# Kernel optimization log

Hardware: AMD Instinct MI355X
Metric: run time of the kernel (lower is better)

## Reference

```python
import jax, jax.numpy as jnp
import numpy as np

NH = 16   # num_heads
HD = 128  # head_dim
HS = 2048 # hidden_size
LI, LT = 2048, 512
MLP = 4 * HS


def _ln(x, s, b):
    m = jnp.mean(x, axis=-1, keepdims=True)
    v = jnp.var(x, axis=-1, keepdims=True)
    return (x - m) * jax.lax.rsqrt(v + 1e-6) * s + b


def _rms(x, s):
    return x * jax.lax.rsqrt(jnp.mean(x * x, axis=-1, keepdims=True) + 1e-6) * s


def _mod6(vec, w, b):
    a = (jax.nn.silu(vec) @ w + b)[:, None, :]
    return jnp.split(a, 6, axis=-1)  # shift1,scale1,gate1,shift2,scale2,gate2


def _rope(x, pe):
    B, H, L, D = x.shape
    xr = x.reshape(B, H, L, D // 2, 1, 2)
    return (pe[..., 0] * xr[..., 0] + pe[..., 1] * xr[..., 1]).reshape(B, H, L, D)


def _attention(q, k, v, pe):
    q = _rope(q, pe)
    k = _rope(k, pe)
    scores = jnp.einsum('bhqd,bhkd->bhqk', q, k) * (q.shape[-1] ** -0.5)
    p = jax.nn.softmax(scores, axis=-1)
    o = jnp.einsum('bhqk,bhkd->bhqd', p, v)
    B, H, L, D = o.shape
    return o.transpose(0, 2, 1, 3).reshape(B, L, H * D)


def _prenorm_qkv(x, shift, scale, ln_s, ln_b, qkv_w, qkv_b, qn, kn):
    xm = (1.0 + scale) * _ln(x, ln_s, ln_b) + shift
    y = xm @ qkv_w + qkv_b
    B, L, _ = y.shape
    y = y.reshape(B, L, 3, NH, HD).transpose(2, 0, 3, 1, 4)  # K B H L D
    q, k, v = y[0], y[1], y[2]
    return _rms(q, qn), _rms(k, kn), v


def _forward(img, txt, vec, pe,
             img_mod_w, img_mod_b, img_norm1_s, img_norm1_b, img_qkv_w, img_qkv_b,
             img_qn_s, img_kn_s, img_proj_w, img_proj_b, img_norm2_s, img_norm2_b,
             img_mlp_w1, img_mlp_b1, img_mlp_w2, img_mlp_b2,
             txt_mod_w, txt_mod_b, txt_norm1_s, txt_norm1_b, txt_qkv_w, txt_qkv_b,
             txt_qn_s, txt_kn_s, txt_proj_w, txt_proj_b, txt_norm2_s, txt_norm2_b,
             txt_mlp_w1, txt_mlp_b1, txt_mlp_w2, txt_mlp_b2):
    i_sh1, i_sc1, i_g1, i_sh2, i_sc2, i_g2 = _mod6(vec, img_mod_w, img_mod_b)
    t_sh1, t_sc1, t_g1, t_sh2, t_sc2, t_g2 = _mod6(vec, txt_mod_w, txt_mod_b)

    iq, ik, iv = _prenorm_qkv(img, i_sh1, i_sc1, img_norm1_s, img_norm1_b,
                              img_qkv_w, img_qkv_b, img_qn_s, img_kn_s)
    tq, tk, tv = _prenorm_qkv(txt, t_sh1, t_sc1, txt_norm1_s, txt_norm1_b,
                              txt_qkv_w, txt_qkv_b, txt_qn_s, txt_kn_s)

    q = jnp.concatenate((tq, iq), axis=2)
    k = jnp.concatenate((tk, ik), axis=2)
    v = jnp.concatenate((tv, iv), axis=2)
    attn = _attention(q, k, v, pe)  # [B, LT+LI, HS]
    Lt = txt.shape[1]
    txt_attn, img_attn = attn[:, :Lt], attn[:, Lt:]

    img = img + i_g1 * (img_attn @ img_proj_w + img_proj_b)
    img_h = (1.0 + i_sc2) * _ln(img, img_norm2_s, img_norm2_b) + i_sh2
    img = img + i_g2 * (jax.nn.gelu(img_h @ img_mlp_w1 + img_mlp_b1) @ img_mlp_w2 + img_mlp_b2)

    txt = txt + t_g1 * (txt_attn @ txt_proj_w + txt_proj_b)
    txt_h = (1.0 + t_sc2) * _ln(txt, txt_norm2_s, txt_norm2_b) + t_sh2
    txt = txt + t_g2 * (jax.nn.gelu(txt_h @ txt_mlp_w1 + txt_mlp_b1) @ txt_mlp_w2 + txt_mlp_b2)
    return img, txt


def setup_inputs() -> dict:
    key = jax.random.key(0)
    ki = iter(jax.random.split(key, 48))
    def n(shape, s=0.02):
        return jax.random.normal(next(ki), shape, jnp.float32) * s
    d = {
        'img': jax.random.normal(next(ki), (1, LI, HS), jnp.float32),
        'txt': jax.random.normal(next(ki), (1, LT, HS), jnp.float32),
        'vec': jax.random.normal(next(ki), (1, HS), jnp.float32),
        'pe': jax.random.normal(next(ki), (1, 1, LT + LI, HD // 2, 2, 2), jnp.float32),
    }
    for p in ('img', 'txt'):
        d[p + '_mod_w'] = n((HS, 6 * HS)); d[p + '_mod_b'] = jnp.zeros((6 * HS,), jnp.float32)
        d[p + '_norm1_s'] = jnp.ones((HS,), jnp.float32); d[p + '_norm1_b'] = jnp.zeros((HS,), jnp.float32)
        d[p + '_qkv_w'] = n((HS, 3 * HS)); d[p + '_qkv_b'] = jnp.zeros((3 * HS,), jnp.float32)
        d[p + '_qn_s'] = jnp.ones((HD,), jnp.float32); d[p + '_kn_s'] = jnp.ones((HD,), jnp.float32)
        d[p + '_proj_w'] = n((HS, HS)); d[p + '_proj_b'] = jnp.zeros((HS,), jnp.float32)
        d[p + '_norm2_s'] = jnp.ones((HS,), jnp.float32); d[p + '_norm2_b'] = jnp.zeros((HS,), jnp.float32)
        d[p + '_mlp_w1'] = n((HS, MLP)); d[p + '_mlp_b1'] = jnp.zeros((MLP,), jnp.float32)
        d[p + '_mlp_w2'] = n((MLP, HS)); d[p + '_mlp_b2'] = jnp.zeros((HS,), jnp.float32)
    return d


def reference(img, txt, vec, pe,
              img_mod_w, img_mod_b, img_norm1_s, img_norm1_b, img_qkv_w, img_qkv_b,
              img_qn_s, img_kn_s, img_proj_w, img_proj_b, img_norm2_s, img_norm2_b,
              img_mlp_w1, img_mlp_b1, img_mlp_w2, img_mlp_b2,
              txt_mod_w, txt_mod_b, txt_norm1_s, txt_norm1_b, txt_qkv_w, txt_qkv_b,
              txt_qn_s, txt_kn_s, txt_proj_w, txt_proj_b, txt_norm2_s, txt_norm2_b,
              txt_mlp_w1, txt_mlp_b1, txt_mlp_w2, txt_mlp_b2):
    return _forward(img, txt, vec, pe,
                    img_mod_w, img_mod_b, img_norm1_s, img_norm1_b, img_qkv_w, img_qkv_b,
                    img_qn_s, img_kn_s, img_proj_w, img_proj_b, img_norm2_s, img_norm2_b,
                    img_mlp_w1, img_mlp_b1, img_mlp_w2, img_mlp_b2,
                    txt_mod_w, txt_mod_b, txt_norm1_s, txt_norm1_b, txt_qkv_w, txt_qkv_b,
                    txt_qn_s, txt_kn_s, txt_proj_w, txt_proj_b, txt_norm2_s, txt_norm2_b,
                    txt_mlp_w1, txt_mlp_b1, txt_mlp_w2, txt_mlp_b2)
```

## Files before the change

kernel.cpp:

```cpp
#include <hip/hip_runtime.h>
#include <hip/hip_bf16.h>
#include <math.h>

typedef __bf16 bf16;
typedef __bf16 bf16x2 __attribute__((ext_vector_type(2)));
typedef __bf16 bf16x4 __attribute__((ext_vector_type(4)));
typedef __bf16 bf16x8 __attribute__((ext_vector_type(8)));
typedef float f32x4 __attribute__((ext_vector_type(4)));

#define HS 2048
#define NH 16
#define HD 128
#define LT 512
#define LI 2048
#define LQ 2560
#define MLP_D 8192
#define SPLIT 4
#define KVS (LQ / SPLIT)
#define KVBLK 32
#define NTILES (KVS / KVBLK)

__device__ __forceinline__ f32x4 mfma16(bf16x8 a, bf16x8 b, f32x4 c) {
  return __builtin_amdgcn_mfma_f32_16x16x32_bf16(a, b, c, 0, 0, 0);
}

__device__ __forceinline__ void gl_lds16(const bf16* g, bf16* l) {
  __builtin_amdgcn_global_load_lds((const __attribute__((address_space(1))) void*)g,
                                   (__attribute__((address_space(3))) void*)l, 16, 0, 0);
}

__global__ void k_silu(const float* __restrict__ v, float* __restrict__ s) {
  int i = blockIdx.x * 256 + threadIdx.x;
  float x = v[i];
  s[i] = x / (1.f + expf(-x));
}

__global__ __launch_bounds__(256) void k_mod_partial(
    const float* __restrict__ s, const float* __restrict__ w_txt,
    const float* __restrict__ w_img, float* __restrict__ part) {
  int strm = blockIdx.x / 48;
  int n = (blockIdx.x % 48) * 256 + threadIdx.x;
  const float* w = strm ? w_img : w_txt;
  int k0 = blockIdx.y * 256;
  __shared__ float sl[256];
  sl[threadIdx.x] = s[k0 + threadIdx.x];
  __syncthreads();
  float acc = 0.f;
  for (int k = 0; k < 256; k++)
    acc += sl[k] * w[(size_t)(k0 + k) * 12288 + n];
  part[((size_t)blockIdx.y * 2 + strm) * 12288 + n] = acc;
}

__global__ __launch_bounds__(256) void k_mod_reduce(
    const float* __restrict__ part, const float* __restrict__ b_txt,
    const float* __restrict__ b_img, float* __restrict__ mod) {
  int strm = blockIdx.x / 48;
  int n = (blockIdx.x % 48) * 256 + threadIdx.x;
  float acc = strm ? b_img[n] : b_txt[n];
  for (int kc = 0; kc < 8; kc++)
    acc += part[((size_t)kc * 2 + strm) * 12288 + n];
  mod[(size_t)strm * 12288 + n] = acc;
}

__global__ __launch_bounds__(256) void k_transpose_cvt(
    const float* __restrict__ src, bf16* __restrict__ dst, int R, int C) {
  __shared__ float t[64][65];
  int tx = threadIdx.x & 63, ty = threadIdx.x >> 6;
  int c0 = blockIdx.x * 64, r0 = blockIdx.y * 64;
  for (int i = 0; i < 64; i += 4)
    t[ty + i][tx] = src[(size_t)(r0 + ty + i) * C + c0 + tx];
  __syncthreads();
#pragma unroll
  for (int j = 0; j < 2; j++) {
    int c = (threadIdx.x >> 3) + j * 32;
    int gg = (threadIdx.x & 7) * 8;
    bf16x8 ov;
#pragma unroll
    for (int k = 0; k < 8; k++) ov[k] = (bf16)t[gg + k][c];
    *(bf16x8*)(dst + (size_t)(c0 + c) * R + r0 + gg) = ov;
  }
}

__global__ __launch_bounds__(256) void k_ln_mod(
    const float* __restrict__ x0, const float* __restrict__ x1,
    const float* __restrict__ ls0, const float* __restrict__ lb0,
    const float* __restrict__ ls1, const float* __restrict__ lb1,
    const float* __restrict__ mod0, const float* __restrict__ mod1,
    int shidx, int scidx, bf16* __restrict__ out) {
  int r = blockIdx.x;
  int strm = r >= LT;
  const float* x = strm ? (x1 + (size_t)(r - LT) * HS) : (x0 + (size_t)r * HS);
  const float* ls = strm ? ls1 : ls0;
  const float* lb = strm ? lb1 : lb0;
  const float* md = strm ? mod1 : mod0;
  const float* sh = md + (size_t)shidx * HS;
  const float* sc = md + (size_t)scidx * HS;
  int t = threadIdx.x;
  float4 a = ((const float4*)x)[t * 2];
  float4 b = ((const float4*)x)[t * 2 + 1];
  float xv[8] = {a.x, a.y, a.z, a.w, b.x, b.y, b.z, b.w};
  float sum = 0.f, sq = 0.f;
#pragma unroll
  for (int j = 0; j < 8; j++) { sum += xv[j]; sq += xv[j] * xv[j]; }
#pragma unroll
  for (int m = 32; m; m >>= 1) { sum += __shfl_xor(sum, m); sq += __shfl_xor(sq, m); }
  __shared__ float red[8];
  int lane = t & 63, wid = t >> 6;
  if (!lane) { red[wid] = sum; red[wid + 4] = sq; }
  __syncthreads();
  float ts = red[0] + red[1] + red[2] + red[3];
  float tq = red[4] + red[5] + red[6] + red[7];
  float mean = ts * (1.f / HS);
  float var = tq * (1.f / HS) - mean * mean;
  float inv = rsqrtf(var + 1e-6f);
  int c0 = t * 8;
  bf16x8 ov;
#pragma unroll
  for (int j = 0; j < 8; j++) {
    int c = c0 + j;
    float v = ((xv[j] - mean) * inv * ls[c] + lb[c]) * (1.f + sc[c]) + sh[c];
    ov[j] = (bf16)v;
  }
  *(bf16x8*)(out + (size_t)r * HS + c0) = ov;
}

template <int MODE>
__global__ __launch_bounds__(256) void k_gemm(
    const bf16* __restrict__ A, int K, int N, int Ksz,
    const bf16* __restrict__ BT0, const bf16* __restrict__ BT1,
    const float* __restrict__ bias0, const float* __restrict__ bias1,
    void* __restrict__ out0, void* __restrict__ out1) {
  __shared__ bf16 As[3][128 * 32];
  __shared__ bf16 Bs[3][128 * 32];
  int tid = threadIdx.x;
  int bn = blockIdx.x, bm = blockIdx.y;
  int strm = (bm * 128) >= LT;
  int lm = bm * 128 - strm * LT;
  const bf16* BT = strm ? BT1 : BT0;
  int lane = tid & 63, wid = tid >> 6;
  int wr = wid >> 1, wc = wid & 1;
  int sc_ = (lane & 7) ^ (lane >> 3);
  int Rb = wid * 16 + 2 * (lane >> 3) + (sc_ >> 2);
  int koff = (sc_ & 3) * 8;
  const bf16* Ag = A + (size_t)(bm * 128 + Rb) * K + koff;
  const bf16* Bg = BT + (size_t)(bn * 128 + Rb) * K + koff;
  int kbeg = MODE == 4 ? blockIdx.z * Ksz : 0;
  int nk = Ksz / 32;
  auto stage = [&](int buf, int ks) {
    int k0 = kbeg + ks * 32;
    gl_lds16(Ag + k0, &As[buf][wid * 512]);
    gl_lds16(Ag + (size_t)64 * K + k0, &As[buf][2048 + wid * 512]);
    gl_lds16(Bg + k0, &Bs[buf][wid * 512]);
    gl_lds16(Bg + (size_t)64 * K + k0, &Bs[buf][2048 + wid * 512]);
  };
  f32x4 acc[4][4] = {};
  int r16 = lane & 15, g = lane >> 4;
  int Lr = r16 >> 1;
  int pf_ = (((r16 & 1) << 2) + g) ^ Lr;
  stage(0, 0);
  if (nk > 1) stage(1, 1);
  int c0 = 0;
  for (int ks = 0; ks < nk; ks++) {
    if (ks + 1 < nk) asm volatile("s_waitcnt vmcnt(4)" ::: "memory");
    else             asm volatile("s_waitcnt vmcnt(0)" ::: "memory");
    __builtin_amdgcn_s_barrier();
    asm volatile("" ::: "memory");
    int c2 = c0 + 2; if (c2 >= 3) c2 -= 3;
    if (ks + 2 < nk) stage(c2, ks + 2);
    bf16x8 af[4], bfr[4];
#pragma unroll
    for (int m = 0; m < 4; m++)
      af[m] = *(const bf16x8*)&As[c0][(wr * 32 + m * 8 + Lr) * 64 + pf_ * 8];
#pragma unroll
    for (int n = 0; n < 4; n++)
      bfr[n] = *(const bf16x8*)&Bs[c0][(wc * 32 + n * 8 + Lr) * 64 + pf_ * 8];
#pragma unroll
    for (int m = 0; m < 4; m++)
#pragma unroll
      for (int n = 0; n < 4; n++)
        acc[m][n] = mfma16(af[m], bfr[n], acc[m][n]);
    c0 = (c0 + 1 == 3) ? 0 : c0 + 1;
  }
  int col = lane & 15, rb = (lane >> 4) * 4;
  const float* bias = strm ? bias1 : bias0;
  float* part = MODE == 4 ? (float*)out0 + (size_t)blockIdx.z * LQ * N : nullptr;
#pragma unroll
  for (int m = 0; m < 4; m++) {
#pragma unroll
    for (int n = 0; n < 4; n++) {
      int gn = bn * 128 + wc * 64 + n * 16 + col;
      float bv = MODE == 4 ? 0.f : bias[gn];
#pragma unroll
      for (int r = 0; r < 4; r++) {
        int lr = wr * 64 + m * 16 + rb + r;
        float v = acc[m][n][r] + bv;
        if (MODE == 0) {
          ((bf16*)(strm ? out1 : out0))[(size_t)(lm + lr) * N + gn] = (bf16)v;
        } else if (MODE == 2) {
          float u2 = 1.5957691216057308f * (v + 0.044715f * v * v * v);
          float ge = v / (1.f + __expf(-u2));
          ((bf16*)(strm ? out1 : out0))[(size_t)(lm + lr) * N + gn] = (bf16)ge;
        } else {
          part[(size_t)(bm * 128 + lr) * N + gn] = v;
        }
      }
    }
  }
}

template <int S>
__global__ __launch_bounds__(256) void k_skcomb(
    const float* __restrict__ part, int N,
    const float* __restrict__ bias0, const float* __restrict__ bias1,
    const float* __restrict__ gate0, const float* __restrict__ gate1,
    const float* __restrict__ res0, const float* __restrict__ res1,
    float* __restrict__ out0, float* __restrict__ out1) {
  int gid = blockIdx.x * 256 + threadIdx.x;
  int nv = N >> 2;
  int row = gid / nv, cv = gid - row * nv;
  int strm = row >= LT;
  int lrow = row - strm * LT;
  const float* bias = strm ? bias1 : bias0;
  const float* gate = strm ? gate1 : gate0;
  const float* res = strm ? res1 : res0;
  float* out = strm ? out1 : out0;
  int c = cv * 4;
  float4 acc = *(const float4*)(bias + c);
#pragma unroll
  for (int s = 0; s < S; s++) {
    float4 p = *(const float4*)(part + ((size_t)s * LQ + row) * N + c);
    acc.x += p.x; acc.y += p.y; acc.z += p.z; acc.w += p.w;
  }
  float4 g = *(const float4*)(gate + c);
  float4 r = *(const float4*)(res + (size_t)lrow * N + c);
  float4 o = {r.x + g.x * acc.x, r.y + g.y * acc.y, r.z + g.z * acc.z, r.w + g.w * acc.w};
  *(float4*)(out + (size_t)lrow * N + c) = o;
}

__global__ __launch_bounds__(256) void k_qkv_post(
    const bf16* __restrict__ y, const float* __restrict__ pe,
    const float* __restrict__ qn0, const float* __restrict__ kn0,
    const float* __restrict__ qn1, const float* __restrict__ kn1,
    bf16* __restrict__ qh, bf16* __restrict__ kh) {
  int wv = (int)((blockIdx.x * 256 + threadIdx.x) >> 6);
  int lane = threadIdx.x & 63;
  int head = wv / LQ, l = wv - head * LQ;
  const bf16* yr = y + (size_t)l * (3 * HS) + head * HD;
  float q0 = (float)yr[2 * lane], q1 = (float)yr[2 * lane + 1];
  float k0 = (float)yr[HS + 2 * lane], k1 = (float)yr[HS + 2 * lane + 1];
  float sqs = q0 * q0 + q1 * q1, sks = k0 * k0 + k1 * k1;
#pragma unroll
  for (int m = 1; m < 64; m <<= 1) { sqs += __shfl_xor(sqs, m); sks += __shfl_xor(sks, m); }
  float rq = rsqrtf(sqs * (1.f / HD) + 1e-6f);
  float rk = rsqrtf(sks * (1.f / HD) + 1e-6f);
  int strm = l >= LT;
  const float* qn = strm ? qn1 : qn0;
  const float* kn = strm ? kn1 : kn0;
  float e0 = q0 * rq * qn[2 * lane], e1 = q1 * rq * qn[2 * lane + 1];
  float f0 = k0 * rk * kn[2 * lane], f1 = k1 * rk * kn[2 * lane + 1];
  float4 p = *(const float4*)(pe + ((size_t)l * 64 + lane) * 4);
  const float scl = 0.12751744f;
  size_t qi = ((size_t)head * LQ + l) * HD + 2 * lane;
  bf16x2 qv = {(bf16)((p.x * e0 + p.y * e1) * scl), (bf16)((p.z * e0 + p.w * e1) * scl)};
  bf16x2 kv = {(bf16)(p.x * f0 + p.y * f1), (bf16)(p.z * f0 + p.w * f1)};
  *(bf16x2*)(qh + qi) = qv;
  *(bf16x2*)(kh + qi) = kv;
}

__global__ __launch_bounds__(256) void k_vtrans(const bf16* __restrict__ y,
                                                bf16* __restrict__ vT) {
  __shared__ bf16 t[32][34];
  int head = blockIdx.y >> 2, dt = blockIdx.y & 3;
  int tx = threadIdx.x & 31, ty = threadIdx.x >> 5;
  int l0 = blockIdx.x * 32, d0 = dt * 32;
  for (int i = 0; i < 32; i += 8)
    t[ty + i][tx] = y[(size_t)(l0 + ty + i) * (3 * HS) + 2 * HS + head * HD + d0 + tx];
  __syncthreads();
  for (int i = 0; i < 32; i += 8)
    vT[(size_t)(head * HD + d0 + ty + i) * LQ + l0 + tx] = t[tx][ty + i];
}

__global__ __launch_bounds__(256, 5) void k_attn(
    const bf16* __restrict__ Q, const bf16* __restrict__ Kh,
    const bf16* __restrict__ VT, bf16* __restrict__ Op, float* __restrict__ ml) {
  __shared__ bf16 Ks[2][KVBLK * 128];
  __shared__ bf16 Vs[2][128 * KVBLK];
  int tid = threadIdx.x, lane = tid & 63, w = tid >> 6;
  int b = blockIdx.x;
  int qb = b % 40;
  int split = (b / 40) % SPLIT;
  int head = b / (40 * SPLIT);
  int qr = qb * 64 + w * 16;
  int r16 = lane & 15, g = lane >> 4;
  const bf16* qp = Q + ((size_t)head * LQ + qr + r16) * HD + g * 8;
  bf16x8 qf[4];
#pragma unroll
  for (int c = 0; c < 4; c++) qf[c] = *(const bf16x8*)(qp + c * 32);
  f32x4 O[8] = {};
  float mr = -1e30f, lr = 0.f;
  const bf16* kbase = Kh + ((size_t)head * LQ + split * KVS) * HD;
  const bf16* vbase = VT + (size_t)head * HD * LQ + split * KVS;
  int krow0 = w * 8 + (lane >> 4);
  int kslot = lane & 15;
  int vc_ = (lane & 7) ^ (lane >> 3);
  int vd0 = w * 32 + 2 * (lane >> 3) + (vc_ >> 2);
  int vkoff = (vc_ & 3) * 8;
  auto stage = [&](int buf, int t) {
    int kv0 = t * KVBLK;
#pragma unroll
    for (int i = 0; i < 2; i++) {
      int krow = krow0 + i * 4;
      gl_lds16(kbase + (size_t)(kv0 + krow) * HD + ((kslot ^ (krow & 7)) << 3),
               &Ks[buf][(w * 8 + i * 4) * 128]);
      gl_lds16(vbase + (size_t)(vd0 + i * 16) * LQ + kv0 + vkoff,
               &Vs[buf][w * 1024 + i * 512]);
    }
  };
  stage(0, 0);
  int cur = 0;
  int src0 = r16 + ((g & 1) << 5);
  bool hiS = g >= 2;
  int LrV = r16 >> 1;
  int pv_ = (((r16 & 1) << 2) + g) ^ LrV;
  for (int t = 0; t < NTILES; t++) {
    __syncthreads();
    if (t + 1 < NTILES) stage(cur ^ 1, t + 1);
    const bf16* ks = &Ks[cur][0];
    const bf16* vs = &Vs[cur][0];
    f32x4 S0 = {}, S1 = {};
    int sw = (r16 & 7);
#pragma unroll
    for (int c = 0; c < 4; c++) {
      int slot = ((4 * c + g) ^ sw) << 3;
      bf16x8 ka = *(const bf16x8*)&ks[r16 * 128 + slot];
      bf16x8 kb = *(const bf16x8*)&ks[(16 + r16) * 128 + slot];
      S0 = mfma16(ka, qf[c], S0);
      S1 = mfma16(kb, qf[c], S1);
    }
    float mx = fmaxf(fmaxf(fmaxf(S0[0], S0[1]), fmaxf(S0[2], S0[3])),
                     fmaxf(fmaxf(S1[0], S1[1]), fmaxf(S1[2], S1[3])));
    mx = fmaxf(mx, __shfl_xor(mx, 16));
    mx = fmaxf(mx, __shfl_xor(mx, 32));
    bool keep = __all(mx <= mr + 8.f);
    float alpha = 1.f;
    if (!keep) {
      float mn = fmaxf(mr, mx);
      alpha = exp2f(mr - mn);
      mr = mn;
    }
    float p0 = exp2f(S0[0] - mr), p1 = exp2f(S0[1] - mr);
    float p2 = exp2f(S0[2] - mr), p3 = exp2f(S0[3] - mr);
    float p4 = exp2f(S1[0] - mr), p5 = exp2f(S1[1] - mr);
    float p6 = exp2f(S1[2] - mr), p7 = exp2f(S1[3] - mr);
    float rs = ((p0 + p1) + (p2 + p3)) + ((p4 + p5) + (p6 + p7));
    rs += __shfl_xor(rs, 16);
    rs += __shfl_xor(rs, 32);
    lr = fmaf(lr, alpha, rs);
    bf16x2 a0 = {(bf16)p0, (bf16)p1}, a1 = {(bf16)p2, (bf16)p3};
    bf16x2 b0 = {(bf16)p4, (bf16)p5}, b1 = {(bf16)p6, (bf16)p7};
    int A0 = *(int*)&a0, A1 = *(int*)&a1, B0 = *(int*)&b0, B1 = *(int*)&b1;
    int x0a = __shfl(A0, src0), x0b = __shfl(B0, src0);
    int x1a = __shfl(A1, src0), x1b = __shfl(B1, src0);
    int x2a = __shfl(A0, src0 + 16), x2b = __shfl(B0, src0 + 16);
    int x3a = __shfl(A1, src0 + 16), x3b = __shfl(B1, src0 + 16);
    union { int u[4]; bf16x8 v; } pu;
    pu.u[0] = hiS ? x0b : x0a;
    pu.u[1] = hiS ? x1b : x1a;
    pu.u[2] = hiS ? x2b : x2a;
    pu.u[3] = hiS ? x3b : x3a;
    bf16x8 pf = pu.v;
    if (!keep) {
#pragma unroll
      for (int n = 0; n < 8; n++) O[n] *= alpha;
    }
#pragma unroll
    for (int n = 0; n < 8; n++) {
      bf16x8 vf = *(const bf16x8*)&vs[(n * 8 + LrV) * 64 + pv_ * 8];
      O[n] = mfma16(vf, pf, O[n]);
    }
    cur ^= 1;
  }
  const int NL = NH * LQ;
  bf16* op = Op + (size_t)split * NL * HD;
  size_t rowbase = ((size_t)head * LQ + qr + r16) * HD + 4 * g;
#pragma unroll
  for (int n = 0; n < 8; n++) {
    bf16x4 ov = {(bf16)O[n][0], (bf16)O[n][1], (bf16)O[n][2], (bf16)O[n][3]};
    *(bf16x4*)(op + rowbase + n * 16) = ov;
  }
  if (g == 0) {
    int idx = head * LQ + qr + r16;
    ml[(size_t)(split * 2 + 0) * NL + idx] = mr;
    ml[(size_t)(split * 2 + 1) * NL + idx] = lr;
  }
}

__global__ __launch_bounds__(256) void k_attn_combine(
    const bf16* __restrict__ Op, const float* __restrict__ ml, bf16* __restrict__ out) {
  int lane = threadIdx.x & 63, w = threadIdx.x >> 6;
  int row = blockIdx.x * 4 + w;
  int head = row / LQ, l = row - head * LQ;
  const int NL = NH * LQ;
  float ms[SPLIT], ls[SPLIT], m = -1e30f;
#pragma unroll
  for (int s = 0; s < SPLIT; s++) {
    ms[s] = ml[(size_t)(s * 2) * NL + row];
    ls[s] = ml[(size_t)(s * 2 + 1) * NL + row];
    m = fmaxf(m, ms[s]);
  }
  float wsum = 0.f, wgt[SPLIT];
#pragma unroll
  for (int s = 0; s < SPLIT; s++) { wgt[s] = exp2f(ms[s] - m); wsum += wgt[s] * ls[s]; }
  float inv = 1.f / wsum;
  size_t oi = (size_t)row * HD + 2 * lane;
  float a0 = 0.f, a1 = 0.f;
#pragma unroll
  for (int s = 0; s < SPLIT; s++) {
    bf16x2 v = *(const bf16x2*)(Op + (size_t)s * NL * HD + oi);
    a0 += wgt[s] * (float)v[0];
    a1 += wgt[s] * (float)v[1];
  }
  bf16x2 ov = {(bf16)(a0 * inv), (bf16)(a1 * inv)};
  *(bf16x2*)(out + (size_t)l * HS + head * HD + 2 * lane) = ov;
}

extern "C" void kernel_launch(void* const* d_in, const int* in_sizes, int n_in,
                              void* d_out, int out_size, void* d_ws, size_t ws_size,
                              hipStream_t stream) {
  const float* img = (const float*)d_in[0];
  const float* txt = (const float*)d_in[1];
  const float* vec = (const float*)d_in[2];
  const float* pe = (const float*)d_in[3];
#define PARAM(i) ((const float*)d_in[i])

  char* ws = (char*)d_ws;
  size_t off = 0;
  auto alloc = [&](size_t b) { void* p = ws + off; off += (b + 255) & ~(size_t)255; return p; };
  float* silu_s = (float*)alloc((size_t)HS * 4);
  float* mpart = (float*)alloc((size_t)8 * 2 * 12288 * 4);
  float* mod = (float*)alloc((size_t)2 * 6 * HS * 4);
  bf16* qkvT0 = (bf16*)alloc((size_t)3 * HS * HS * 2);
  bf16* qkvT1 = (bf16*)alloc((size_t)3 * HS * HS * 2);
  bf16* projT0 = (bf16*)alloc((size_t)HS * HS * 2);
  bf16* projT1 = (bf16*)alloc((size_t)HS * HS * 2);
  bf16* mlp1T0 = (bf16*)alloc((size_t)MLP_D * HS * 2);
  bf16* mlp1T1 = (bf16*)alloc((size_t)MLP_D * HS * 2);
  bf16* mlp2T0 = (bf16*)alloc((size_t)HS * MLP_D * 2);
  bf16* mlp2T1 = (bf16*)alloc((size_t)HS * MLP_D * 2);
  bf16* xm = (bf16*)alloc((size_t)LQ * HS * 2);
  bf16* y = (bf16*)alloc((size_t)LQ * 3 * HS * 2);
  bf16* qh = (bf16*)alloc((size_t)NH * LQ * HD * 2);
  bf16* kh = (bf16*)alloc((size_t)NH * LQ * HD * 2);
  bf16* vT = (bf16*)alloc((size_t)NH * HD * LQ * 2);
  bf16* attnb = (bf16*)alloc((size_t)LQ * HS * 2);
  float* x2 = (float*)alloc((size_t)LQ * HS * 4);
  bf16* xm2 = (bf16*)alloc((size_t)LQ * HS * 2);
  bf16* h = (bf16*)alloc((size_t)LQ * MLP_D * 2);
  float* ml = (float*)alloc((size_t)2 * SPLIT * NH * LQ * 4);
  bf16* Op = h;
  float* skpart = (float*)xm;
  (void)ws_size; (void)in_sizes; (void)n_in; (void)out_size;

  const float* t_mod = mod;
  const float* i_mod = mod + 6 * HS;

  k_silu<<<HS / 256, 256, 0, stream>>>(vec, silu_s);
  k_mod_partial<<<dim3(96, 8), 256, 0, stream>>>(silu_s, PARAM(20), PARAM(4), mpart);
  k_mod_reduce<<<96, 256, 0, stream>>>(mpart, PARAM(21), PARAM(5), mod);

  k_transpose_cvt<<<dim3(3 * HS / 64, HS / 64), 256, 0, stream>>>(PARAM(24), qkvT0, HS, 3 * HS);
  k_transpose_cvt<<<dim3(3 * HS / 64, HS / 64), 256, 0, stream>>>(PARAM(8), qkvT1, HS, 3 * HS);
  k_transpose_cvt<<<dim3(HS / 64, HS / 64), 256, 0, stream>>>(PARAM(28), projT0, HS, HS);
  k_transpose_cvt<<<dim3(HS / 64, HS / 64), 256, 0, stream>>>(PARAM(12), projT1, HS, HS);
  k_transpose_cvt<<<dim3(MLP_D / 64, HS / 64), 256, 0, stream>>>(PARAM(32), mlp1T0, HS, MLP_D);
  k_transpose_cvt<<<dim3(MLP_D / 64, HS / 64), 256, 0, stream>>>(PARAM(16), mlp1T1, HS, MLP_D);
  k_transpose_cvt<<<dim3(HS / 64, MLP_D / 64), 256, 0, stream>>>(PARAM(34), mlp2T0, MLP_D, HS);
  k_transpose_cvt<<<dim3(HS / 64, MLP_D / 64), 256, 0, stream>>>(PARAM(18), mlp2T1, MLP_D, HS);

  k_ln_mod<<<LQ, 256, 0, stream>>>(txt, img, PARAM(22), PARAM(23), PARAM(6), PARAM(7),
                                   t_mod, i_mod, 0, 1, xm);

  k_gemm<0><<<dim3(3 * HS / 128, LQ / 128), 256, 0, stream>>>(
      xm, HS, 3 * HS, HS, qkvT0, qkvT1, PARAM(25), PARAM(9), y, y + (size_t)LT * 3 * HS);

  k_qkv_post<<<NH * LQ / 4, 256, 0, stream>>>(y, pe, PARAM(26), PARAM(27), PARAM(10), PARAM(11),
                                              qh, kh);
  k_vtrans<<<dim3(LQ / 32, NH * 4), 256, 0, stream>>>(y, vT);

  k_attn<<<NH * SPLIT * 40, 256, 0, stream>>>(qh, kh, vT, Op, ml);
  k_attn_combine<<<NH * LQ / 4, 256, 0, stream>>>(Op, ml, attnb);

  k_gemm<4><<<dim3(HS / 128, LQ / 128, 2), 256, 0, stream>>>(
      attnb, HS, HS, HS / 2, projT0, projT1, nullptr, nullptr, skpart, nullptr);
  k_skcomb<2><<<LQ * HS / 4 / 256, 256, 0, stream>>>(
      skpart, HS, PARAM(29), PARAM(13), t_mod + 2 * HS, i_mod + 2 * HS, txt, img,
      x2, x2 + (size_t)LT * HS);

  k_ln_mod<<<LQ, 256, 0, stream>>>(x2, x2 + (size_t)LT * HS, PARAM(30), PARAM(31), PARAM(14),
                                   PARAM(15), t_mod, i_mod, 3, 4, xm2);

  k_gemm<2><<<dim3(MLP_D / 128, LQ / 128), 256, 0, stream>>>(
      xm2, HS, MLP_D, HS, mlp1T0, mlp1T1, PARAM(33), PARAM(17), h, h + (size_t)LT * MLP_D);

  float* out_img = (float*)d_out;
  float* out_txt = (float*)d_out + (size_t)LI * HS;
  k_gemm<4><<<dim3(HS / 128, LQ / 128, 4), 256, 0, stream>>>(
      h, MLP_D, HS, MLP_D / 4, mlp2T0, mlp2T1, nullptr, nullptr, skpart, nullptr);
  k_skcomb<4><<<LQ * HS / 4 / 256, 256, 0, stream>>>(
      skpart, HS, PARAM(35), PARAM(19), t_mod + 5 * HS, i_mod + 5 * HS, x2,
      x2 + (size_t)LT * HS, out_txt, out_img);
}
```

Measured before the change: 756.0 us.

## Widen attention query tile, fuse residual-combine with LayerNorm, batch transposes

The attention kernel now handles 32 query rows per wave instead of 16, so each K/V tile in LDS feeds twice the MFMA work. This halves the block count, and launch bounds drop to 2 blocks per SM to make room for the extra registers. The post-projection split-K combine is fused with the second LN/modulation kernel, saving one round trip of x2 through memory. Weight transposes for the two streams are batched into single launches via blockIdx.z, and the MLP2 GEMM split-K factor goes from 4 to 2, which trades fewer partial sums for less parallelism.

```diff
diff --git a/kernel.cpp b/kernel.cpp
--- a/kernel.cpp
+++ b/kernel.cpp
@@ -62,8 +62,11 @@
   mod[(size_t)strm * 12288 + n] = acc;
 }
 
-__global__ __launch_bounds__(256) void k_transpose_cvt(
-    const float* __restrict__ src, bf16* __restrict__ dst, int R, int C) {
+__global__ __launch_bounds__(256) void k_transpose_cvt2(
+    const float* __restrict__ s0, const float* __restrict__ s1,
+    bf16* __restrict__ d0, bf16* __restrict__ d1, int R, int C) {
+  const float* src = blockIdx.z ? s1 : s0;
+  bf16* dst = blockIdx.z ? d1 : d0;
   __shared__ float t[64][65];
   int tx = threadIdx.x & 63, ty = threadIdx.x >> 6;
   int c0 = blockIdx.x * 64, r0 = blockIdx.y * 64;
@@ -237,6 +240,67 @@
   *(float4*)(out + (size_t)lrow * N + c) = o;
 }
 
+__global__ __launch_bounds__(256) void k_skcomb_ln(
+    const float* __restrict__ part,
+    const float* __restrict__ pb0, const float* __restrict__ pb1,
+    const float* __restrict__ gate0, const float* __restrict__ gate1,
+    const float* __restrict__ res0, const float* __restrict__ res1,
+    const float* __restrict__ ls0, const float* __restrict__ lb0,
+    const float* __restrict__ ls1, const float* __restrict__ lb1,
+    const float* __restrict__ mod0, const float* __restrict__ mod1,
+    float* __restrict__ x2, bf16* __restrict__ xm2) {
+  int r = blockIdx.x;
+  int strm = r >= LT;
+  int lrow = r - strm * LT;
+  const float* bias = strm ? pb1 : pb0;
+  const float* gate = strm ? gate1 : gate0;
+  const float* res = (strm ? res1 : res0) + (size_t)lrow * HS;
+  const float* ls = strm ? ls1 : ls0;
+  const float* lb = strm ? lb1 : lb0;
+  const float* md = strm ? mod1 : mod0;
+  const float* sh = md + 3 * HS;
+  const float* sc = md + 4 * HS;
+  int t = threadIdx.x, c0 = t * 8;
+  float vv[8];
+#pragma unroll
+  for (int j = 0; j < 2; j++) {
+    float4 p0 = *(const float4*)(part + (size_t)r * HS + c0 + 4 * j);
+    float4 p1 = *(const float4*)(part + ((size_t)LQ + r) * HS + c0 + 4 * j);
+    float4 bi = *(const float4*)(bias + c0 + 4 * j);
+    float4 gt = *(const float4*)(gate + c0 + 4 * j);
+    float4 rs = *(const float4*)(res + c0 + 4 * j);
+    float4 o;
+    o.x = rs.x + gt.x * (p0.x + p1.x + bi.x);
+    o.y = rs.y + gt.y * (p0.y + p1.y + bi.y);
+    o.z = rs.z + gt.z * (p0.z + p1.z + bi.z);
+    o.w = rs.w + gt.w * (p0.w + p1.w + bi.w);
+    *(float4*)(x2 + (size_t)r * HS + c0 + 4 * j) = o;
+    vv[4 * j + 0] = o.x; vv[4 * j + 1] = o.y; vv[4 * j + 2] = o.z; vv[4 * j + 3] = o.w;
+  }
+  float sum = 0.f, sq = 0.f;
+#pragma unroll
+  for (int j = 0; j < 8; j++) { sum += vv[j]; sq += vv[j] * vv[j]; }
+#pragma unroll
+  for (int m = 32; m; m >>= 1) { sum += __shfl_xor(sum, m); sq += __shfl_xor(sq, m); }
+  __shared__ float red[8];
+  int lane = t & 63, wid = t >> 6;
+  if (!lane) { red[wid] = sum; red[wid + 4] = sq; }
+  __syncthreads();
+  float ts = red[0] + red[1] + red[2] + red[3];
+  float tq = red[4] + red[5] + red[6] + red[7];
+  float mean = ts * (1.f / HS);
+  float var = tq * (1.f / HS) - mean * mean;
+  float inv = rsqrtf(var + 1e-6f);
+  bf16x8 ov;
+#pragma unroll
+  for (int j = 0; j < 8; j++) {
+    int c = c0 + j;
+    float v = ((vv[j] - mean) * inv * ls[c] + lb[c]) * (1.f + sc[c]) + sh[c];
+    ov[j] = (bf16)v;
+  }
+  *(bf16x8*)(xm2 + (size_t)r * HS + c0) = ov;
+}
+
 __global__ __launch_bounds__(256) void k_qkv_post(
     const bf16* __restrict__ y, const float* __restrict__ pe,
     const float* __restrict__ qn0, const float* __restrict__ kn0,
@@ -280,24 +344,28 @@
     vT[(size_t)(head * HD + d0 + ty + i) * LQ + l0 + tx] = t[tx][ty + i];
 }
 
-__global__ __launch_bounds__(256, 5) void k_attn(
+__global__ __launch_bounds__(256, 2) void k_attn(
     const bf16* __restrict__ Q, const bf16* __restrict__ Kh,
     const bf16* __restrict__ VT, bf16* __restrict__ Op, float* __restrict__ ml) {
   __shared__ bf16 Ks[2][KVBLK * 128];
   __shared__ bf16 Vs[2][128 * KVBLK];
   int tid = threadIdx.x, lane = tid & 63, w = tid >> 6;
   int b = blockIdx.x;
-  int qb = b % 40;
-  int split = (b / 40) % SPLIT;
-  int head = b / (40 * SPLIT);
-  int qr = qb * 64 + w * 16;
+  int qb = b % 20;
+  int split = (b / 20) % SPLIT;
+  int head = b / (20 * SPLIT);
+  int qr = qb * 128 + w * 32;
   int r16 = lane & 15, g = lane >> 4;
-  const bf16* qp = Q + ((size_t)head * LQ + qr + r16) * HD + g * 8;
-  bf16x8 qf[4];
-#pragma unroll
-  for (int c = 0; c < 4; c++) qf[c] = *(const bf16x8*)(qp + c * 32);
-  f32x4 O[8] = {};
-  float mr = -1e30f, lr = 0.f;
+  const bf16* qpa = Q + ((size_t)head * LQ + qr + r16) * HD + g * 8;
+  const bf16* qpb = qpa + (size_t)16 * HD;
+  bf16x8 qfa[4], qfb[4];
+#pragma unroll
+  for (int c = 0; c < 4; c++) {
+    qfa[c] = *(const bf16x8*)(qpa + c * 32);
+    qfb[c] = *(const bf16x8*)(qpb + c * 32);
+  }
+  f32x4 Oa[8] = {}, Ob[8] = {};
+  float mra = -1e30f, lra = 0.f, mrb = -1e30f, lrb = 0.f;
   const bf16* kbase = Kh + ((size_t)head * LQ + split * KVS) * HD;
   const bf16* vbase = VT + (size_t)head * HD * LQ + split * KVS;
   int krow0 = w * 8 + (lane >> 4);
@@ -322,27 +390,14 @@
   bool hiS = g >= 2;
   int LrV = r16 >> 1;
   int pv_ = (((r16 & 1) << 2) + g) ^ LrV;
-  for (int t = 0; t < NTILES; t++) {
-    __syncthreads();
-    if (t + 1 < NTILES) stage(cur ^ 1, t + 1);
-    const bf16* ks = &Ks[cur][0];
-    const bf16* vs = &Vs[cur][0];
-    f32x4 S0 = {}, S1 = {};
-    int sw = (r16 & 7);
-#pragma unroll
-    for (int c = 0; c < 4; c++) {
-      int slot = ((4 * c + g) ^ sw) << 3;
-      bf16x8 ka = *(const bf16x8*)&ks[r16 * 128 + slot];
-      bf16x8 kb = *(const bf16x8*)&ks[(16 + r16) * 128 + slot];
-      S0 = mfma16(ka, qf[c], S0);
-      S1 = mfma16(kb, qf[c], S1);
-    }
+  auto smpack = [&](f32x4 S0, f32x4 S1, float& mr, float& lr, float& alpha,
+                    bool& keep) -> bf16x8 {
     float mx = fmaxf(fmaxf(fmaxf(S0[0], S0[1]), fmaxf(S0[2], S0[3])),
                      fmaxf(fmaxf(S1[0], S1[1]), fmaxf(S1[2], S1[3])));
     mx = fmaxf(mx, __shfl_xor(mx, 16));
     mx = fmaxf(mx, __shfl_xor(mx, 32));
-    bool keep = __all(mx <= mr + 8.f);
-    float alpha = 1.f;
+    keep = __all(mx <= mr + 8.f);
+    alpha = 1.f;
     if (!keep) {
       float mn = fmaxf(mr, mx);
       alpha = exp2f(mr - mn);
@@ -368,30 +423,62 @@
     pu.u[1] = hiS ? x1b : x1a;
     pu.u[2] = hiS ? x2b : x2a;
     pu.u[3] = hiS ? x3b : x3a;
-    bf16x8 pf = pu.v;
-    if (!keep) {
-#pragma unroll
-      for (int n = 0; n < 8; n++) O[n] *= alpha;
+    return pu.v;
+  };
+  for (int t = 0; t < NTILES; t++) {
+    __syncthreads();
+    if (t + 1 < NTILES) stage(cur ^ 1, t + 1);
+    const bf16* ks = &Ks[cur][0];
+    const bf16* vs = &Vs[cur][0];
+    f32x4 S0a = {}, S1a = {}, S0b = {}, S1b = {};
+    int sw = (r16 & 7);
+#pragma unroll
+    for (int c = 0; c < 4; c++) {
+      int slot = ((4 * c + g) ^ sw) << 3;
+      bf16x8 ka = *(const bf16x8*)&ks[r16 * 128 + slot];
+      bf16x8 kb = *(const bf16x8*)&ks[(16 + r16) * 128 + slot];
+      S0a = mfma16(ka, qfa[c], S0a);
+      S1a = mfma16(kb, qfa[c], S1a);
+      S0b = mfma16(ka, qfb[c], S0b);
+      S1b = mfma16(kb, qfb[c], S1b);
+    }
+    float alphaa, alphab;
+    bool keepa, keepb;
+    bf16x8 pfa = smpack(S0a, S1a, mra, lra, alphaa, keepa);
+    bf16x8 pfb = smpack(S0b, S1b, mrb, lrb, alphab, keepb);
+    if (!keepa) {
+#pragma unroll
+      for (int n = 0; n < 8; n++) Oa[n] *= alphaa;
+    }
+    if (!keepb) {
+#pragma unroll
+      for (int n = 0; n < 8; n++) Ob[n] *= alphab;
     }
 #pragma unroll
     for (int n = 0; n < 8; n++) {
       bf16x8 vf = *(const bf16x8*)&vs[(n * 8 + LrV) * 64 + pv_ * 8];
-      O[n] = mfma16(vf, pf, O[n]);
+      Oa[n] = mfma16(vf, pfa, Oa[n]);
+      Ob[n] = mfma16(vf, pfb, Ob[n]);
     }
     cur ^= 1;
   }
   const int NL = NH * LQ;
   bf16* op = Op + (size_t)split * NL * HD;
-  size_t rowbase = ((size_t)head * LQ + qr + r16) * HD + 4 * g;
+  size_t rowa = ((size_t)head * LQ + qr + r16) * HD + 4 * g;
+  size_t rowb = rowa + (size_t)16 * HD;
 #pragma unroll
   for (int n = 0; n < 8; n++) {
-    bf16x4 ov = {(bf16)O[n][0], (bf16)O[n][1], (bf16)O[n][2], (bf16)O[n][3]};
-    *(bf16x4*)(op + rowbase + n * 16) = ov;
+    bf16x4 ova = {(bf16)Oa[n][0], (bf16)Oa[n][1], (bf16)Oa[n][2], (bf16)Oa[n][3]};
+    bf16x4 ovb = {(bf16)Ob[n][0], (bf16)Ob[n][1], (bf16)Ob[n][2], (bf16)Ob[n][3]};
+    *(bf16x4*)(op + rowa + n * 16) = ova;
+    *(bf16x4*)(op + rowb + n * 16) = ovb;
   }
   if (g == 0) {
-    int idx = head * LQ + qr + r16;
-    ml[(size_t)(split * 2 + 0) * NL + idx] = mr;
-    ml[(size_t)(split * 2 + 1) * NL + idx] = lr;
+    int idxa = head * LQ + qr + r16;
+    ml[(size_t)(split * 2 + 0) * NL + idxa] = mra;
+    ml[(size_t)(split * 2 + 1) * NL + idxa] = lra;
+    ml[(size_t)(split * 2 + 0) * NL + idxa + 16] = mrb;
+    ml[(size_t)(split * 2 + 1) * NL + idxa + 16] = lrb;
   }
 }
 
@@ -468,14 +555,14 @@
   k_mod_partial<<<dim3(96, 8), 256, 0, stream>>>(silu_s, PARAM(20), PARAM(4), mpart);
   k_mod_reduce<<<96, 256, 0, stream>>>(mpart, PARAM(21), PARAM(5), mod);
 
-  k_transpose_cvt<<<dim3(3 * HS / 64, HS / 64), 256, 0, stream>>>(PARAM(24), qkvT0, HS, 3 * HS);
-  k_transpose_cvt<<<dim3(3 * HS / 64, HS / 64), 256, 0, stream>>>(PARAM(8), qkvT1, HS, 3 * HS);
-  k_transpose_cvt<<<dim3(HS / 64, HS / 64), 256, 0, stream>>>(PARAM(28), projT0, HS, HS);
-  k_transpose_cvt<<<dim3(HS / 64, HS / 64), 256, 0, stream>>>(PARAM(12), projT1, HS, HS);
-  k_transpose_cvt<<<dim3(MLP_D / 64, HS / 64), 256, 0, stream>>>(PARAM(32), mlp1T0, HS, MLP_D);
-  k_transpose_cvt<<<dim3(MLP_D / 64, HS / 64), 256, 0, stream>>>(PARAM(16), mlp1T1, HS, MLP_D);
-  k_transpose_cvt<<<dim3(HS / 64, MLP_D / 64), 256, 0, stream>>>(PARAM(34), mlp2T0, MLP_D, HS);
-  k_transpose_cvt<<<dim3(HS / 64, MLP_D / 64), 256, 0, stream>>>(PARAM(18), mlp2T1, MLP_D, HS);
+  k_transpose_cvt2<<<dim3(3 * HS / 64, HS / 64, 2), 256, 0, stream>>>(
+      PARAM(24), PARAM(8), qkvT0, qkvT1, HS, 3 * HS);
+  k_transpose_cvt2<<<dim3(HS / 64, HS / 64, 2), 256, 0, stream>>>(
+      PARAM(28), PARAM(12), projT0, projT1, HS, HS);
+  k_transpose_cvt2<<<dim3(MLP_D / 64, HS / 64, 2), 256, 0, stream>>>(
+      PARAM(32), PARAM(16), mlp1T0, mlp1T1, HS, MLP_D);
+  k_transpose_cvt2<<<dim3(HS / 64, MLP_D / 64, 2), 256, 0, stream>>>(
+      PARAM(34), PARAM(18), mlp2T0, mlp2T1, MLP_D, HS);
 
   k_ln_mod<<<LQ, 256, 0, stream>>>(txt, img, PARAM(22), PARAM(23), PARAM(6), PARAM(7),
                                    t_mod, i_mod, 0, 1, xm);
@@ -487,26 +574,23 @@
                                               qh, kh);
   k_vtrans<<<dim3(LQ / 32, NH * 4), 256, 0, stream>>>(y, vT);
 
-  k_attn<<<NH * SPLIT * 40, 256, 0, stream>>>(qh, kh, vT, Op, ml);
+  k_attn<<<NH * SPLIT * 20, 256, 0, stream>>>(qh, kh, vT, Op, ml);
   k_attn_combine<<<NH * LQ / 4, 256, 0, stream>>>(Op, ml, attnb);
 
   k_gemm<4><<<dim3(HS / 128, LQ / 128, 2), 256, 0, stream>>>(
       attnb, HS, HS, HS / 2, projT0, projT1, nullptr, nullptr, skpart, nullptr);
-  k_skcomb<2><<<LQ * HS / 4 / 256, 256, 0, stream>>>(
-      skpart, HS, PARAM(29), PARAM(13), t_mod + 2 * HS, i_mod + 2 * HS, txt, img,
-      x2, x2 + (size_t)LT * HS);
-
-  k_ln_mod<<<LQ, 256, 0, stream>>>(x2, x2 + (size_t)LT * HS, PARAM(30), PARAM(31), PARAM(14),
-                                   PARAM(15), t_mod, i_mod, 3, 4, xm2);
+  k_skcomb_ln<<<LQ, 256, 0, stream>>>(
+      skpart, PARAM(29), PARAM(13), t_mod + 2 * HS, i_mod + 2 * HS, txt, img,
+      PARAM(30), PARAM(31), PARAM(14), PARAM(15), t_mod, i_mod, x2, xm2);
 
   k_gemm<2><<<dim3(MLP_D / 128, LQ / 128), 256, 0, stream>>>(
       xm2, HS, MLP_D, HS, mlp1T0, mlp1T1, PARAM(33), PARAM(17), h, h + (size_t)LT * MLP_D);
 
   float* out_img = (float*)d_out;
   float* out_txt = (float*)d_out + (size_t)LI * HS;
-  k_gemm<4><<<dim3(HS / 128, LQ / 128, 4), 256, 0, stream>>>(
-      h, MLP_D, HS, MLP_D / 4, mlp2T0, mlp2T1, nullptr, nullptr, skpart, nullptr);
-  k_skcomb<4><<<LQ * HS / 4 / 256, 256, 0, stream>>>(
+  k_gemm<4><<<dim3(HS / 128, LQ / 128, 2), 256, 0, stream>>>(
+      h, MLP_D, HS, MLP_D / 2, mlp2T0, mlp2T1, nullptr, nullptr, skpart, nullptr);
+  k_skcomb<2><<<LQ * HS / 4 / 256, 256, 0, stream>>>(
       skpart, HS, PARAM(35), PARAM(19), t_mod + 5 * HS, i_mod + 5 * HS, x2,
       x2 + (size_t)LT * HS, out_txt, out_img);
 }
```

After: 736.1 us. 1.03x faster.
